# Kernel optimization log

Measured on AMD Instinct MI355X. Metric: run time of the kernel, lower is better.

## Reference

```python
import jax, jax.numpy as jnp
import numpy as np

TAU = 0.1
K = 60.0
CHUNK = 64
B = 1024


def setup_inputs() -> dict:
    key = jax.random.key(0)
    k1, k2, k3, k4 = jax.random.split(key, 4)
    s_v = jax.random.normal(k1, (B, B), jnp.float32)
    s_l = jax.random.normal(k2, (B, B), jnp.float32)
    # class-label based positive/negative masks (typical metric-learning batch)
    labels = jax.random.randint(k3, (B,), 0, B // 8)
    pos_mask = labels[:, None] == labels[None, :]
    neg_mask = ~pos_mask
    w_v = jax.random.uniform(k4, (B, B), jnp.float32)
    w_l = 1.0 - w_v
    return dict(s_v=s_v, s_l=s_l, pos_mask=pos_mask, neg_mask=neg_mask, w_v=w_v, w_l=w_l)


def _soft_ranks(sim, pos_f, neg_f, tau=TAU, chunk=CHUNK):
    """Row-chunked differentiable soft ranks. sim/pos_f/neg_f: [B, B] float."""
    b = sim.shape[0]
    nc = b // chunk  # B divisible by chunk

    def body(args):
        cs, cp, cn = args                                   # [chunk, B] each
        # sig[c, k, j] = sigmoid((s_ck - s_cj) / tau)
        sig = jax.nn.sigmoid((cs[:, :, None] - cs[:, None, :]) / tau)
        rank_pos = 1.0 + jnp.einsum('ckj,ck->cj', sig, cn)  # count negatives above
        rank_neg = 1.0 + jnp.einsum('ckj,ck->cj', sig, cp)  # count positives above
        return rank_pos * cp + rank_neg * cn

    args = (sim.reshape(nc, chunk, b), pos_f.reshape(nc, chunk, b), neg_f.reshape(nc, chunk, b))
    return jax.lax.map(jax.checkpoint(body), args).reshape(b, b)


def reference(s_v, s_l, pos_mask, neg_mask, w_v, w_l):
    pos_f = pos_mask.astype(s_v.dtype)
    neg_f = neg_mask.astype(s_v.dtype)
    rank_v = _soft_ranks(s_v, pos_f, neg_f)
    rank_l = _soft_ranks(s_l, pos_f, neg_f)
    S_hat = (K + 1.0) * (w_v / (K + rank_v) + w_l / (K + rank_l))
    return S_hat
```

## Files before the change

kernel.cpp:

```cpp
#include <hip/hip_runtime.h>


#define NB 1024
#define CEXP 14.426950408889634f
#define SCL  0.000030517578125f
#define NBUK 128
#define BUK0 4.3f
#define BUKW 14.883720930f
#define DBUK 2
#define CHSZ 128
#define NJOB 32
#define MAXPOS 64
#define ECLMP 1e17f

__device__ __forceinline__ float fma_sat(float a, float b, float c) {
    float d;
    asm("v_fma_f32 %0, %1, %2, %3 clamp" : "=v"(d) : "v"(a), "v"(b), "v"(c));
    return d;
}

__device__ __forceinline__ float nrcp(float d) {
    float r = __uint_as_float(0x7EF311C3u - __float_as_uint(d));
    r = r * fmaf(-d, r, 2.0f);
    return r;
}

#define TREE(Es, ra, rb, A)                                      \
    {                                                            \
        const float y1 = fma_sat((Es), (ra).x, SCL);             \
        const float y2 = fma_sat((Es), (ra).y, SCL);             \
        const float y3 = fma_sat((Es), (ra).z, SCL);             \
        const float y4 = fma_sat((Es), (ra).w, SCL);             \
        const float y5 = fma_sat((Es), (rb).x, SCL);             \
        const float y6 = fma_sat((Es), (rb).y, SCL);             \
        const float y7 = fma_sat((Es), (rb).z, SCL);             \
        const float y8 = fma_sat((Es), (rb).w, SCL);             \
        const float p12 = y1 * y2, p34 = y3 * y4;                \
        const float p56 = y5 * y6, p78 = y7 * y8;                \
        const float s12 = y1 + y2, s34 = y3 + y4;                \
        const float s56 = y5 + y6, s78 = y7 + y8;                \
        const float q1 = p12 * p34, q2 = p56 * p78;              \
        const float n1 = fmaf(s12, p34, s34 * p12);              \
        const float n2 = fmaf(s56, p78, s78 * p56);              \
        const float num = fmaf(n1, q2, n2 * q1);                 \
        const float den = q1 * q2;                               \
        (A) = fmaf(num, nrcp(den), (A));                         \
    }

__global__ __launch_bounds__(512) void drank_kernel(
    const float* __restrict__ s_v, const float* __restrict__ s_l,
    const unsigned char* __restrict__ pos_m,
    const unsigned char* __restrict__ neg_m,
    const float* __restrict__ w_v, const float* __restrict__ w_l,
    float* __restrict__ out)
{
    __shared__ float  listRv[NB], listRl[NB];
    __shared__ int    listJv[NB], listJl[NB];
    __shared__ float  sAv1[NB], sAl1[NB];
    __shared__ float  sAv2[NB], sAl2[NB];
    __shared__ int    offv[NBUK + 1], offl[NBUK + 1];
    __shared__ float  SRv[129], SEv[129];
    __shared__ float  SR2v[129], SE2v[129];
    __shared__ float  SRl[129], SEl[129];
    __shared__ float  SR2l[129], SE2l[129];
    __shared__ float2 posR[MAXPOS];
    __shared__ int    npos_s, jobCtr;

    int* curv = (int*)sAv1;
    int* curl = (int*)sAl1;

    const int c = blockIdx.x;
    const int t = threadIdx.x;
    const long row = (long)c * NB;

    if (t < NBUK) { curv[t] = 0; curl[t] = 0; }
    if (t == 0) { npos_s = 0; jobCtr = 0; }
    __syncthreads();

    const unsigned int W =
        ((const unsigned int*)pos_m)[0] ^ ((const unsigned int*)neg_m)[0];
    const int mode = (W == 0x01010101u) ? 0 : ((W == 0x3f800000u) ? 2 : 1);

    const int j0 = t * 2;
    const float2 sjv = *(const float2*)(s_v + row + j0);
    const float2 sjl = *(const float2*)(s_l + row + j0);
    const float svu[2] = {sjv.x, sjv.y};
    const float slu[2] = {sjl.x, sjl.y};

    float Rv[2], Rl[2], Ev[2], El[2];
    int ibv[2], ibl[2];
    #pragma unroll
    for (int u = 0; u < 2; ++u) {
        Rv[u] = __builtin_amdgcn_exp2f(-svu[u] * CEXP);
        Rl[u] = __builtin_amdgcn_exp2f(-slu[u] * CEXP);
        Ev[u] = __builtin_amdgcn_exp2f(svu[u] * CEXP);
        El[u] = __builtin_amdgcn_exp2f(slu[u] * CEXP);
        ibv[u] = max(0, min(NBUK - 1, (int)((svu[u] + BUK0) * BUKW)));
        ibl[u] = max(0, min(NBUK - 1, (int)((slu[u] + BUK0) * BUKW)));
        atomicAdd(&curv[ibv[u]], 1);
        atomicAdd(&curl[ibl[u]], 1);
    }

    bool pj[2];
    if (mode == 0) {
        const unsigned short b = ((const unsigned short*)pos_m)[(row >> 1) + t];
        pj[0] = (b & 0x00ffu) != 0; pj[1] = (b & 0xff00u) != 0;
    } else if (mode == 2) {
        const float2 p = *(const float2*)((const float*)pos_m + row + j0);
        pj[0] = p.x != 0.f; pj[1] = p.y != 0.f;
    } else {
        const int2 p = *(const int2*)((const int*)pos_m + row + j0);
        pj[0] = p.x != 0; pj[1] = p.y != 0;
    }
    #pragma unroll
    for (int u = 0; u < 2; ++u) {
        if (pj[u]) {
            const int idx = atomicAdd(&npos_s, 1);
            if (idx < MAXPOS) posR[idx] = make_float2(Rv[u], Rl[u]);
        }
    }
    __syncthreads();

    if (t < 128) {
        const int m = t >> 6, l = t & 63;
        int* cnt = m ? curl : curv;
        int* off = m ? offl : offv;
        const int c0 = cnt[2 * l], c1 = cnt[2 * l + 1];
        int s = c0 + c1;
        #pragma unroll
        for (int d = 1; d < 64; d <<= 1) {
            const int y = __shfl_up(s, d, 64);
            if (l >= d) s += y;
        }
        const int excl = s - c0 - c1;
        off[2 * l] = excl;     off[2 * l + 1] = excl + c0;
        cnt[2 * l] = excl;     cnt[2 * l + 1] = excl + c0;
        if (l == 63) off[NBUK] = s;
    }
    __syncthreads();

    #pragma unroll
    for (int u = 0; u < 2; ++u) {
        const int pv = atomicAdd(&curv[ibv[u]], 1);
        listRv[pv] = Rv[u];
        listJv[pv] = (j0 + u) | (ibv[u] << 16);
        const int pl = atomicAdd(&curl[ibl[u]], 1);
        listRl[pl] = Rl[u];
        listJl[pl] = (j0 + u) | (ibl[u] << 16);
    }
    __syncthreads();

    {
        const int wid = t >> 6, l = t & 63;
        const int m   = (wid >> 1) & 1;
        const int fE  = wid & 1;
        const int sq  = wid >> 2;
        const float4* L4 = (const float4*)(m ? listRl : listRv);
        float* arr;
        switch (wid) {
            case 0: arr = SRv;  break;  case 1: arr = SEv;  break;
            case 2: arr = SRl;  break;  case 3: arr = SEl;  break;
            case 4: arr = SR2v; break;  case 5: arr = SE2v; break;
            case 6: arr = SR2l; break;  default: arr = SE2l; break;
        }
        const int o0 = fE ? (2 * l) : (127 - 2 * l);
        const int o1 = fE ? (2 * l + 1) : (126 - 2 * l);
        float s01[2];
        #pragma unroll
        for (int q = 0; q < 2; ++q) {
            const int o = q ? o1 : o0;
            const float4 a = L4[2 * o], b = L4[2 * o + 1];
            float x[8] = {a.x, a.y, a.z, a.w, b.x, b.y, b.z, b.w};
            float acc = 0.f;
            #pragma unroll
            for (int i = 0; i < 8; ++i) {
                float v = fE ? __builtin_amdgcn_rcpf(x[i]) : x[i];
                v = fminf(v, ECLMP);
                acc += sq ? v * v : v;
            }
            s01[q] = acc;
        }
        float s = s01[0] + s01[1];
        #pragma unroll
        for (int d = 1; d < 64; d <<= 1) {
            const float y = __shfl_up(s, d, 64);
            if (l >= d) s += y;
        }
        if (fE) {
            const float excl = s - s01[0] - s01[1];
            arr[o0] = excl;  arr[o1] = excl + s01[0];
            if (l == 63) arr[128] = s;
        } else {
            arr[o1] = s;  arr[o0] = s - s01[1];
            if (l == 0) arr[128] = 0.f;
        }
    }
    __syncthreads();

    static const unsigned char CORD[8] = {3, 4, 2, 5, 1, 6, 0, 7};
    const int lane = t & 63;

    for (;;) {
        int jid0 = 0;
        if (lane == 0) jid0 = atomicAdd(&jobCtr, 1);
        const int jid = __builtin_amdgcn_readfirstlane(jid0);
        if (jid >= NJOB) break;
        const int ch = CORD[jid >> 2];
        const int m  = (jid >> 1) & 1;
        const int h  = jid & 1;

        const float*  LR  = m ? listRl : listRv;
        const int*    LJ  = m ? listJl : listJv;
        const int*    off = m ? offl : offv;
        float*        SA  = h ? (m ? sAl2 : sAv2) : (m ? sAl1 : sAv1);
        const float*  SR  = m ? SRl : SRv;
        const float*  SE  = m ? SEl : SEv;
        const float*  SR2 = m ? SR2l : SR2v;
        const float*  SE2 = m ? SE2l : SE2v;
        const float4* L4  = (const float4*)LR;

        const int p0 = ch * CHSZ + 2 * lane;
        const float2 R2 = *(const float2*)(LR + p0);
        const int2   jj = *(const int2*)(LJ + p0);
        const float Ex = __builtin_amdgcn_rcpf(R2.x);
        const float Ey = __builtin_amdgcn_rcpf(R2.y);
        const float EsX = SCL * Ex;
        const float EsY = SCL * Ey;

        const int bs = LJ[ch * CHSZ] >> 16;
        const int be = LJ[ch * CHSZ + CHSZ - 1] >> 16;
        const int lo0 = off[max(0, bs - DBUK)] & ~7;
        const int hi0 = (off[min(NBUK - 1, be + DBUK) + 1] + 7) & ~7;
        const int mid = ((lo0 + hi0) >> 1) & ~7;
        const int lo = h ? mid : lo0;
        const int hi = h ? hi0 : mid;

        float a0 = 0.f, a1 = 0.f;
        #pragma unroll 2
        for (int p = lo; p < hi; p += 8) {
            const float4 ra = L4[p >> 2];
            const float4 rb = L4[(p >> 2) + 1];
            TREE(EsX, ra, rb, a0);
            TREE(EsY, ra, rb, a1);
        }
        float cx, cy;
        if (h) {
            const float sr = SR[hi0 >> 3], sr2 = SR2[hi0 >> 3];
            const float Exc = fminf(Ex, ECLMP), Eyc = fminf(Ey, ECLMP);
            cx = (float)(NB - hi0) - Exc * sr + (Exc * Exc) * sr2;
            cy = (float)(NB - hi0) - Eyc * sr + (Eyc * Eyc) * sr2;
        } else {
            const float se = SE[lo0 >> 3], se2 = SE2[lo0 >> 3];
            const float Rxc = fminf(R2.x, ECLMP), Ryc = fminf(R2.y, ECLMP);
            cx = Rxc * se - (Rxc * Rxc) * se2;
            cy = Ryc * se - (Ryc * Ryc) * se2;
        }
        SA[jj.x & 0xFFFF] = fmaf(a0, SCL, cx);
        SA[jj.y & 0xFFFF] = fmaf(a1, SCL, cy);
    }

    float sPv[2] = {0.f, 0.f};
    float sPl[2] = {0.f, 0.f};
    const int np = min(npos_s, MAXPOS);
    for (int i = 0; i < np; ++i) {
        const float2 rp = posR[i];
        #pragma unroll
        for (int u = 0; u < 2; ++u) {
            sPv[u] += __builtin_amdgcn_rcpf(fmaf(Ev[u], rp.x, 1.0f));
            sPl[u] += __builtin_amdgcn_rcpf(fmaf(El[u], rp.y, 1.0f));
        }
    }
    __syncthreads();

    const float2 av1 = *(const float2*)(sAv1 + j0);
    const float2 av2 = *(const float2*)(sAv2 + j0);
    const float2 al1 = *(const float2*)(sAl1 + j0);
    const float2 al2 = *(const float2*)(sAl2 + j0);
    const float sAvu[2] = {av1.x + av2.x, av1.y + av2.y};
    const float sAlu[2] = {al1.x + al2.x, al1.y + al2.y};
    const float2 wv = *(const float2*)(w_v + row + j0);
    const float2 wl = *(const float2*)(w_l + row + j0);
    const float wva[2] = {wv.x, wv.y};
    const float wla[2] = {wl.x, wl.y};
    float o[2];
    #pragma unroll
    for (int u = 0; u < 2; ++u) {
        const float rv = pj[u] ? (1.0f + sAvu[u] - sPv[u]) : (1.0f + sPv[u]);
        const float rl = pj[u] ? (1.0f + sAlu[u] - sPl[u]) : (1.0f + sPl[u]);
        o[u] = 61.0f * (wva[u] / (60.0f + rv) + wla[u] / (60.0f + rl));
    }
    float2 o2;
    o2.x = o[0]; o2.y = o[1];
    *(float2*)(out + row + j0) = o2;
}

extern "C" void kernel_launch(void* const* d_in, const int* in_sizes, int n_in,
                              void* d_out, int out_size, void* d_ws, size_t ws_size,
                              hipStream_t stream) {
    const float* s_v = (const float*)d_in[0];
    const float* s_l = (const float*)d_in[1];
    const unsigned char* pos_m = (const unsigned char*)d_in[2];
    const unsigned char* neg_m = (const unsigned char*)d_in[3];
    const float* w_v = (const float*)d_in[4];
    const float* w_l = (const float*)d_in[5];
    float* out = (float*)d_out;

    drank_kernel<<<dim3(NB), dim3(512), 0, stream>>>(s_v, s_l, pos_m, neg_m, w_v, w_l, out);
}
```

Baseline: 117.2 us.

## Refine buckets and add cubic tail correction to soft-rank sigmoid sums

Doubles the bucket count to 256 with a narrower width and widens the exact window to three buckets. Adds a third-order term to the series approximation of the sigmoid tails, which needs new prefix-sum tables of cubed values. The two half-job accumulation arrays are merged into one buffer updated with shared-memory atomics, zeroed by otherwise idle threads. The aim is to shrink the exact-evaluation window per chunk while keeping accuracy, at the cost of more prefix scans, extra tail arithmetic and atomic adds.

```diff
diff --git a/kernel.cpp b/kernel.cpp
--- a/kernel.cpp
+++ b/kernel.cpp
@@ -4,14 +4,15 @@
 #define NB 1024
 #define CEXP 14.426950408889634f
 #define SCL  0.000030517578125f
-#define NBUK 128
+#define NBUK 256
 #define BUK0 4.3f
-#define BUKW 14.883720930f
-#define DBUK 2
+#define BUKW 29.767441860f
+#define DBUK 3
 #define CHSZ 128
 #define NJOB 32
 #define MAXPOS 64
-#define ECLMP 1e17f
+#define CLMP1 1e17f
+#define CLMP3 5e11f
 
 __device__ __forceinline__ float fma_sat(float a, float b, float c) {
     float d;
@@ -56,18 +57,19 @@
 {
     __shared__ float  listRv[NB], listRl[NB];
     __shared__ int    listJv[NB], listJl[NB];
-    __shared__ float  sAv1[NB], sAl1[NB];
-    __shared__ float  sAv2[NB], sAl2[NB];
+    __shared__ float  sAv[NB], sAl[NB];
     __shared__ int    offv[NBUK + 1], offl[NBUK + 1];
-    __shared__ float  SRv[129], SEv[129];
+    __shared__ float  SRv[129],  SEv[129];
     __shared__ float  SR2v[129], SE2v[129];
-    __shared__ float  SRl[129], SEl[129];
+    __shared__ float  SR3v[129], SE3v[129];
+    __shared__ float  SRl[129],  SEl[129];
     __shared__ float  SR2l[129], SE2l[129];
+    __shared__ float  SR3l[129], SE3l[129];
     __shared__ float2 posR[MAXPOS];
     __shared__ int    npos_s, jobCtr;
 
-    int* curv = (int*)sAv1;
-    int* curl = (int*)sAl1;
+    int* curv = (int*)sAv;
+    int* curl = (int*)sAl;
 
     const int c = blockIdx.x;
     const int t = threadIdx.x;
@@ -125,16 +127,20 @@
         const int m = t >> 6, l = t & 63;
         int* cnt = m ? curl : curv;
         int* off = m ? offl : offv;
-        const int c0 = cnt[2 * l], c1 = cnt[2 * l + 1];
-        int s = c0 + c1;
+        const int c0 = cnt[4 * l], c1 = cnt[4 * l + 1];
+        const int c2 = cnt[4 * l + 2], c3 = cnt[4 * l + 3];
+        int s = c0 + c1 + c2 + c3;
         #pragma unroll
         for (int d = 1; d < 64; d <<= 1) {
             const int y = __shfl_up(s, d, 64);
             if (l >= d) s += y;
         }
-        const int excl = s - c0 - c1;
-        off[2 * l] = excl;     off[2 * l + 1] = excl + c0;
-        cnt[2 * l] = excl;     cnt[2 * l + 1] = excl + c0;
+        const int e0 = s - c0 - c1 - c2 - c3;
+        const int e1 = e0 + c0, e2 = e1 + c1, e3 = e2 + c2;
+        off[4 * l] = e0; off[4 * l + 1] = e1;
+        off[4 * l + 2] = e2; off[4 * l + 3] = e3;
+        cnt[4 * l] = e0; cnt[4 * l + 1] = e1;
+        cnt[4 * l + 2] = e2; cnt[4 * l + 3] = e3;
         if (l == 63) off[NBUK] = s;
     }
     __syncthreads();
@@ -150,50 +156,59 @@
     }
     __syncthreads();
 
-    {
+    if (t < 256) {
         const int wid = t >> 6, l = t & 63;
-        const int m   = (wid >> 1) & 1;
-        const int fE  = wid & 1;
-        const int sq  = wid >> 2;
+        const int m  = wid >> 1;
+        const int fE = wid & 1;
         const float4* L4 = (const float4*)(m ? listRl : listRv);
-        float* arr;
-        switch (wid) {
-            case 0: arr = SRv;  break;  case 1: arr = SEv;  break;
-            case 2: arr = SRl;  break;  case 3: arr = SEl;  break;
-            case 4: arr = SR2v; break;  case 5: arr = SE2v; break;
-            case 6: arr = SR2l; break;  default: arr = SE2l; break;
-        }
+        float* A1 = m ? (fE ? SEl : SRl)   : (fE ? SEv : SRv);
+        float* A2 = m ? (fE ? SE2l : SR2l) : (fE ? SE2v : SR2v);
+        float* A3 = m ? (fE ? SE3l : SR3l) : (fE ? SE3v : SR3v);
         const int o0 = fE ? (2 * l) : (127 - 2 * l);
         const int o1 = fE ? (2 * l + 1) : (126 - 2 * l);
-        float s01[2];
+        float p1[2], p2[2], p3[2];
         #pragma unroll
         for (int q = 0; q < 2; ++q) {
             const int o = q ? o1 : o0;
             const float4 a = L4[2 * o], b = L4[2 * o + 1];
-            float x[8] = {a.x, a.y, a.z, a.w, b.x, b.y, b.z, b.w};
-            float acc = 0.f;
+            const float x[8] = {a.x, a.y, a.z, a.w, b.x, b.y, b.z, b.w};
+            float s1 = 0.f, s2 = 0.f, s3 = 0.f;
             #pragma unroll
             for (int i = 0; i < 8; ++i) {
-                float v = fE ? __builtin_amdgcn_rcpf(x[i]) : x[i];
-                v = fminf(v, ECLMP);
-                acc += sq ? v * v : v;
+                const float v  = fE ? __builtin_amdgcn_rcpf(x[i]) : x[i];
+                const float v1 = fminf(v, CLMP1);
+                const float v3 = fminf(v, CLMP3);
+                s1 += v1;
+                s2 = fmaf(v1, v1, s2);
+                s3 = fmaf(v3 * v3, v3, s3);
             }
-            s01[q] = acc;
-        }
-        float s = s01[0] + s01[1];
-        #pragma unroll
-        for (int d = 1; d < 64; d <<= 1) {
-            const float y = __shfl_up(s, d, 64);
-            if (l >= d) s += y;
-        }
-        if (fE) {
-            const float excl = s - s01[0] - s01[1];
-            arr[o0] = excl;  arr[o1] = excl + s01[0];
-            if (l == 63) arr[128] = s;
-        } else {
-            arr[o1] = s;  arr[o0] = s - s01[1];
-            if (l == 0) arr[128] = 0.f;
-        }
+            p1[q] = s1; p2[q] = s2; p3[q] = s3;
+        }
+#define SCAN2(P, ARR)                                            \
+        {                                                        \
+            float s = (P)[0] + (P)[1];                           \
+            _Pragma("unroll")                                    \
+            for (int d = 1; d < 64; d <<= 1) {                   \
+                const float y = __shfl_up(s, d, 64);             \
+                if (l >= d) s += y;                              \
+            }                                                    \
+            if (fE) {                                            \
+                const float e = s - (P)[0] - (P)[1];             \
+                ARR[o0] = e; ARR[o1] = e + (P)[0];               \
+                if (l == 63) ARR[128] = s;                       \
+            } else {                                             \
+                ARR[o1] = s; ARR[o0] = s - (P)[1];               \
+                if (l == 0) ARR[128] = 0.f;                      \
+            }                                                    \
+        }
+        SCAN2(p1, A1);
+        SCAN2(p2, A2);
+        SCAN2(p3, A3);
+    } else {
+        const int z = (t - 256) * 4;
+        const float4 z4 = {0.f, 0.f, 0.f, 0.f};
+        *(float4*)(sAv + z) = z4;
+        *(float4*)(sAl + z) = z4;
     }
     __syncthreads();
 
@@ -212,11 +227,13 @@
         const float*  LR  = m ? listRl : listRv;
         const int*    LJ  = m ? listJl : listJv;
         const int*    off = m ? offl : offv;
-        float*        SA  = h ? (m ? sAl2 : sAv2) : (m ? sAl1 : sAv1);
+        float*        SA  = m ? sAl : sAv;
         const float*  SR  = m ? SRl : SRv;
         const float*  SE  = m ? SEl : SEv;
         const float*  SR2 = m ? SR2l : SR2v;
         const float*  SE2 = m ? SE2l : SE2v;
+        const float*  SR3 = m ? SR3l : SR3v;
+        const float*  SE3 = m ? SE3l : SE3v;
         const float4* L4  = (const float4*)LR;
 
         const int p0 = ch * CHSZ + 2 * lane;
@@ -245,18 +262,22 @@
         }
         float cx, cy;
         if (h) {
-            const float sr = SR[hi0 >> 3], sr2 = SR2[hi0 >> 3];
-            const float Exc = fminf(Ex, ECLMP), Eyc = fminf(Ey, ECLMP);
-            cx = (float)(NB - hi0) - Exc * sr + (Exc * Exc) * sr2;
-            cy = (float)(NB - hi0) - Eyc * sr + (Eyc * Eyc) * sr2;
+            const float sr = SR[hi0 >> 3], sr2 = SR2[hi0 >> 3], sr3 = SR3[hi0 >> 3];
+            const float Ex1 = fminf(Ex, CLMP1), Ey1 = fminf(Ey, CLMP1);
+            const float Ex3 = fminf(Ex, CLMP3), Ey3 = fminf(Ey, CLMP3);
+            cx = (float)(NB - hi0) - Ex1 * sr + (Ex1 * Ex1) * sr2
+                 - ((Ex3 * Ex3) * Ex3) * sr3;
+            cy = (float)(NB - hi0) - Ey1 * sr + (Ey1 * Ey1) * sr2
+                 - ((Ey3 * Ey3) * Ey3) * sr3;
         } else {
-            const float se = SE[lo0 >> 3], se2 = SE2[lo0 >> 3];
-            const float Rxc = fminf(R2.x, ECLMP), Ryc = fminf(R2.y, ECLMP);
-            cx = Rxc * se - (Rxc * Rxc) * se2;
-            cy = Ryc * se - (Ryc * Ryc) * se2;
-        }
-        SA[jj.x & 0xFFFF] = fmaf(a0, SCL, cx);
-        SA[jj.y & 0xFFFF] = fmaf(a1, SCL, cy);
+            const float se = SE[lo0 >> 3], se2 = SE2[lo0 >> 3], se3 = SE3[lo0 >> 3];
+            const float Rx1 = fminf(R2.x, CLMP1), Ry1 = fminf(R2.y, CLMP1);
+            const float Rx3 = fminf(R2.x, CLMP3), Ry3 = fminf(R2.y, CLMP3);
+            cx = Rx1 * se - (Rx1 * Rx1) * se2 + ((Rx3 * Rx3) * Rx3) * se3;
+            cy = Ry1 * se - (Ry1 * Ry1) * se2 + ((Ry3 * Ry3) * Ry3) * se3;
+        }
+        atomicAdd(&SA[jj.x & 0xFFFF], fmaf(a0, SCL, cx));
+        atomicAdd(&SA[jj.y & 0xFFFF], fmaf(a1, SCL, cy));
     }
 
     float sPv[2] = {0.f, 0.f};
@@ -272,12 +293,10 @@
     }
     __syncthreads();
 
-    const float2 av1 = *(const float2*)(sAv1 + j0);
-    const float2 av2 = *(const float2*)(sAv2 + j0);
-    const float2 al1 = *(const float2*)(sAl1 + j0);
-    const float2 al2 = *(const float2*)(sAl2 + j0);
-    const float sAvu[2] = {av1.x + av2.x, av1.y + av2.y};
-    const float sAlu[2] = {al1.x + al2.x, al1.y + al2.y};
+    const float2 av = *(const float2*)(sAv + j0);
+    const float2 al = *(const float2*)(sAl + j0);
+    const float sAvu[2] = {av.x, av.y};
+    const float sAlu[2] = {al.x, al.y};
     const float2 wv = *(const float2*)(w_v + row + j0);
     const float2 wl = *(const float2*)(w_l + row + j0);
     const float wva[2] = {wv.x, wv.y};
```

After: 124.6 us. 1.06x slower.
